# Optimization experiments

Measured on AMD Instinct MI355X. Metric: run time of the kernel, lower is better.

## Reference

```python
import jax, jax.numpy as jnp
import numpy as np
import math

B_, V_, D_, N_, H_, W_ = 4, 8, 64, 16, 32, 32
V_LIST = [0.0, 45.0, 90.0, 135.0, 180.0, 225.0, 270.0, 315.0]
GROUPS = 4
EPS = 1e-5


def _make_sample_coords():
    # Replicates F.affine_grid(align_corners=False) for fixed rotation matrices,
    # then maps normalized grid coords to input pixel coords as grid_sample does.
    xs = (np.arange(W_) + 0.5) * 2.0 / W_ - 1.0
    ys = (np.arange(H_) + 0.5) * 2.0 / H_ - 1.0
    X, Y = np.meshgrid(xs, ys)  # (H, W)
    ix_list, iy_list = [], []
    for w in V_LIST:
        a = math.radians(-w)
        c, s = math.cos(a), math.sin(a)
        gx = c * X - s * Y  # theta = [[c,-s,0],[s,c,0]]
        gy = s * X + c * Y
        ix_list.append((gx + 1.0) * W_ / 2.0 - 0.5)
        iy_list.append((gy + 1.0) * H_ / 2.0 - 0.5)
    return (jnp.asarray(np.stack(ix_list), jnp.float32),
            jnp.asarray(np.stack(iy_list), jnp.float32))

IX, IY = _make_sample_coords()  # each (V, H, W)


def _bilinear(sv, iy, ix):
    # sv: (B, D, N, H, W); iy, ix: (H, W) float sampling coords (pixel space)
    x0 = jnp.floor(ix)
    y0 = jnp.floor(iy)
    wx1 = ix - x0
    wy1 = iy - y0

    def corner(yc, xc, wgt):
        m = (yc >= 0) & (yc < H_) & (xc >= 0) & (xc < W_)  # zeros padding
        yi = jnp.clip(yc, 0, H_ - 1).astype(jnp.int32)
        xi = jnp.clip(xc, 0, W_ - 1).astype(jnp.int32)
        return sv[..., yi, xi] * jnp.where(m, wgt, 0.0)

    return (corner(y0, x0, (1.0 - wy1) * (1.0 - wx1))
            + corner(y0, x0 + 1.0, (1.0 - wy1) * wx1)
            + corner(y0 + 1.0, x0, wy1 * (1.0 - wx1))
            + corner(y0 + 1.0, x0 + 1.0, wy1 * wx1))

# vmap over the velocity axis V of s_prev and the per-velocity grids
_transport = jax.vmap(_bilinear, in_axes=(1, 0, 0), out_axes=1)


def _conv(x, w, b=None):
    y = jax.lax.conv_general_dilated(x, w, (1, 1), 'SAME',
                                     dimension_numbers=('NCHW', 'OIHW', 'NCHW'))
    if b is not None:
        y = y + b[None, :, None, None]
    return y


def _group_norm(x, w, b):
    Bn, D, H, W = x.shape
    xg = x.reshape(Bn, GROUPS, D // GROUPS, H, W)
    mu = xg.mean(axis=(2, 3, 4), keepdims=True)
    var = xg.var(axis=(2, 3, 4), keepdims=True)
    xn = ((xg - mu) * jax.lax.rsqrt(var + EPS)).reshape(Bn, D, H, W)
    return xn * w[None, :, None, None] + b[None, :, None, None]


def setup_inputs() -> dict:
    key = jax.random.key(0)
    ks = jax.random.split(key, 5)
    return {
        "u_t": jax.random.normal(ks[0], (B_, D_, H_, W_), jnp.float32),
        "s_prev": jax.random.normal(ks[1], (B_, V_, D_, N_, H_, W_), jnp.float32) * 0.1,
        "gn_w": jnp.ones((D_,), jnp.float32),
        "gn_b": jnp.zeros((D_,), jnp.float32),
        "conv_delta_w": jax.random.normal(ks[2], (D_, D_, 3, 3), jnp.float32) * 0.02,
        "conv_delta_b": jnp.zeros((D_,), jnp.float32),
        "conv_B_w": jax.random.normal(ks[3], (N_, D_, 3, 3), jnp.float32) * 0.02,
        "conv_C_w": jax.random.normal(ks[4], (N_, D_, 3, 3), jnp.float32) * 0.02,
        "log_A_real": jnp.full((D_, N_), math.log(0.5), jnp.float32),
        "D_param": jnp.ones((D_,), jnp.float32),
        "dt_bias": jnp.float32(math.log(math.e - 1.0)),
    }


def reference(u_t, s_prev, gn_w, gn_b, conv_delta_w, conv_delta_b,
              conv_B_w, conv_C_w, log_A_real, D_param, dt_bias):
    u_norm = _group_norm(u_t, gn_w, gn_b)
    delta = jax.nn.softplus(_conv(u_norm, conv_delta_w, conv_delta_b) + dt_bias)
    delta = jnp.clip(delta, 1e-4, 5.0)                               # (B,D,H,W)
    B_val = _conv(u_norm, conv_B_w)                                  # (B,N,H,W)
    C_val = _conv(u_norm, conv_C_w)                                  # (B,N,H,W)
    A = -jnp.exp(log_A_real)                                         # (D,N)
    A_bar = jnp.exp(delta[:, :, None] * A[None, :, :, None, None])   # (B,D,N,H,W)
    B_bar = delta[:, :, None] * B_val[:, None]                       # (B,D,N,H,W)
    s_trans = _transport(s_prev, IY, IX)                             # (B,V,D,N,H,W)
    s_new = A_bar[:, None] * s_trans + B_bar[:, None] * u_t[:, None, :, None]
    y_state = jnp.einsum('bvdnhw,bnhw->bvdhw', s_new, C_val)
    y_new = y_state + u_t[:, None] * D_param[None, None, :, None, None]
    return (y_new, s_new)
```

## Files before the change

kernel.cpp:

```cpp
#include <hip/hip_runtime.h>
#include <cmath>

#define FSQ 0.70710678118654752440f
__constant__ float CTAB[8] = {1.f,  FSQ, 0.f, -FSQ, -1.f, -FSQ, 0.f, FSQ};
__constant__ float STAB[8] = {0.f, -FSQ, -1.f, -FSQ,  0.f,  FSQ, 1.f, FSQ};

typedef float f4 __attribute__((ext_vector_type(4)));

__global__ __launch_bounds__(1024) void gn_kernel(const float* __restrict__ u,
                                                  const float* __restrict__ gw,
                                                  const float* __restrict__ gb,
                                                  float* __restrict__ up)
{
    int blk = blockIdx.x;
    int b = blk >> 2, g = blk & 3;
    int t = threadIdx.x;
    const float* src = u + ((size_t)(b * 64 + g * 16) << 10);
    float sum = 0.f, sq = 0.f;
    #pragma unroll
    for (int r = 0; r < 16; ++r) {
        float v = src[t + (r << 10)];
        sum += v; sq += v * v;
    }
    #pragma unroll
    for (int ofs = 32; ofs > 0; ofs >>= 1) {
        sum += __shfl_down(sum, ofs);
        sq  += __shfl_down(sq, ofs);
    }
    __shared__ float red[16], red2[16];
    int wv = t >> 6;
    if ((t & 63) == 0) { red[wv] = sum; red2[wv] = sq; }
    __syncthreads();
    float s_tot = 0.f, q_tot = 0.f;
    #pragma unroll
    for (int k = 0; k < 16; ++k) { s_tot += red[k]; q_tot += red2[k]; }
    float mu  = s_tot * (1.f / 16384.f);
    float var = q_tot * (1.f / 16384.f) - mu * mu;
    float rs  = rsqrtf(var + 1e-5f);

    float* pb = up + (size_t)(b * 64 + g * 16) * 1156;
    for (int k = t; k < 16 * 132; k += 1024) {
        int pl = k / 132, c = k - pl * 132;
        int idx;
        if (c < 34)       idx = c;
        else if (c < 68)  idx = 33 * 34 + (c - 34);
        else if (c < 100) idx = (c - 68 + 1) * 34;
        else              idx = (c - 100 + 1) * 34 + 33;
        pb[pl * 1156 + idx] = 0.f;
    }
    int y = t >> 5, x = t & 31;
    #pragma unroll
    for (int r = 0; r < 16; ++r) {
        float val = (src[t + (r << 10)] - mu) * rs * gw[g * 16 + r] + gb[g * 16 + r];
        pb[r * 1156 + (y + 1) * 34 + (x + 1)] = val;
    }
}

__global__ __launch_bounds__(256) void conv_kernel(const float* __restrict__ up,
                                                   const float* __restrict__ wd,
                                                   const float* __restrict__ bd,
                                                   const float* __restrict__ wB,
                                                   const float* __restrict__ wC,
                                                   const float* __restrict__ dtb,
                                                   float* __restrict__ delta,
                                                   float* __restrict__ Bv,
                                                   float* __restrict__ Cv)
{
    __shared__ float sin_[64 * 204];
    int blk = blockIdx.x;
    int strip = blk & 7;
    int og = (blk >> 3) % 24;
    int b = blk / 192;
    int h0 = strip * 4;
    int t = threadIdx.x;

    const float* plane = up + (size_t)b * 73984;
    for (int idx = t; idx < 13056; idx += 256) {
        int ci = idx / 204;
        int rem = idx - ci * 204;
        sin_[idx] = plane[ci * 1156 + h0 * 34 + rem];
    }
    __syncthreads();

    int o0 = og * 4;
    const float* wsel;
    if (o0 < 64)      wsel = wd + (size_t)o0 * 576;
    else if (o0 < 80) wsel = wB + (size_t)(o0 - 64) * 576;
    else              wsel = wC + (size_t)(o0 - 80) * 576;

    int half = t >> 7;
    int px = t & 127;
    int r = px >> 5, c = px & 31;
    const float* base = sin_ + r * 34 + c;

    float acc0 = 0.f, acc1 = 0.f, acc2 = 0.f, acc3 = 0.f;
    int ci0 = half * 32;
    for (int ci = ci0; ci < ci0 + 32; ++ci) {
        const float* pp = base + ci * 204;
        const float* wp = wsel + ci * 9;
        #pragma unroll
        for (int dy = 0; dy < 3; ++dy)
            #pragma unroll
            for (int dx = 0; dx < 3; ++dx) {
                float v = pp[dy * 34 + dx];
                int wi = dy * 3 + dx;
                acc0 += v * wp[wi];
                acc1 += v * wp[576 + wi];
                acc2 += v * wp[1152 + wi];
                acc3 += v * wp[1728 + wi];
            }
    }
    __syncthreads();
    float4* red4 = (float4*)sin_;
    red4[t] = make_float4(acc0, acc1, acc2, acc3);
    __syncthreads();
    if (t < 128) {
        float4 a = red4[t], bq = red4[t + 128];
        float s0 = a.x + bq.x, s1 = a.y + bq.y, s2 = a.z + bq.z, s3 = a.w + bq.w;
        float s[4] = {s0, s1, s2, s3};
        int pidx = (h0 + r) * 32 + c;
        if (o0 < 64) {
            #pragma unroll
            for (int k = 0; k < 4; ++k) {
                float x = s[k] + bd[o0 + k] + dtb[0];
                float sp = (x > 20.f) ? x : log1pf(expf(x));
                sp = fminf(fmaxf(sp, 1e-4f), 5.f);
                delta[((size_t)(b * 64 + o0 + k) << 10) + pidx] = sp;
            }
        } else if (o0 < 80) {
            #pragma unroll
            for (int k = 0; k < 4; ++k)
                Bv[((size_t)(b * 16 + o0 - 64 + k) << 10) + pidx] = s[k];
        } else {
            #pragma unroll
            for (int k = 0; k < 4; ++k)
                Cv[((size_t)(b * 16 + o0 - 80 + k) << 10) + pidx] = s[k];
        }
    }
}

__global__ __launch_bounds__(256) void fused_state_kernel(
    const float* __restrict__ s_prev, const float* __restrict__ u_t,
    const float* __restrict__ delta, const float* __restrict__ Bv,
    const float* __restrict__ Cv, const float* __restrict__ logA,
    const float* __restrict__ Dp, float* __restrict__ y_out,
    float* __restrict__ s_out)
{
    __shared__ float lds[4 * 1190];
    __shared__ float Ash[4];
    int blk = blockIdx.x;
    int cchunk = blk >> 11;
    int rest = blk & 2047;
    int d = rest & 63, v = (rest >> 6) & 7, b = rest >> 9;
    int t = threadIdx.x;

    if (t < 4) Ash[t] = -__expf(logA[d * 16 + cchunk * 4 + t]);
    for (int k = t; k < 528; k += 256) {
        int pl = k / 132, g = k - pl * 132;
        int idx;
        if (g < 34)       idx = g;
        else if (g < 68)  idx = 33 * 35 + (g - 34);
        else if (g < 100) idx = (g - 67) * 35;
        else              idx = (g - 99) * 35 + 33;
        lds[pl * 1190 + idx] = 0.f;
    }

    size_t so = (((size_t)((b * 8 + v) * 64 + d)) << 14) + ((size_t)cchunk << 12);
    const float4* src = (const float4*)(s_prev + so);
    #pragma unroll
    for (int k = 0; k < 4; ++k) {
        int q = t + (k << 8);
        float4 val = src[q];
        int lin = q << 2;
        int nn = lin >> 10, rem = lin & 1023;
        int di = nn * 1190 + ((rem >> 5) + 1) * 35 + (rem & 31) + 1;
        lds[di] = val.x; lds[di + 1] = val.y; lds[di + 2] = val.z; lds[di + 3] = val.w;
    }
    __syncthreads();

    const float cc = CTAB[v], ss = STAB[v];
    const f4* dpl4 = (const f4*)(delta + ((size_t)(b * 64 + d) << 10));
    const f4* upl4 = (const f4*)(u_t   + ((size_t)(b * 64 + d) << 10));
    const f4* bvc4 = (const f4*)(Bv + ((size_t)b << 14) + (cchunk << 12));
    const f4* cvc4 = (const f4*)(Cv + ((size_t)b << 14) + (cchunk << 12));
    f4* soc4   = (f4*)(s_out + so);
    float* yo  = y_out + (((size_t)((b * 8 + v) * 64 + d)) << 10);
    float Dd = Dp[d];

    f4 dd4 = dpl4[t], uv4 = upl4[t];

    int h = t >> 3;
    float Yc = (h + 0.5f) * 0.0625f - 1.f;
    float w00[4], w01[4], w10[4], w11[4], duv[4], yacc[4];
    int tb[4];
    #pragma unroll
    for (int j = 0; j < 4; ++j) {
        int wpx = ((t & 7) << 2) | j;
        float X = (wpx + 0.5f) * 0.0625f - 1.f;
        float gx = cc * X - ss * Yc;
        float gy = ss * X + cc * Yc;
        float ix = (gx + 1.f) * 16.f - 0.5f;
        float iy = (gy + 1.f) * 16.f - 0.5f;
        float fx0 = floorf(ix), fy0 = floorf(iy);
        float wx = ix - fx0, wy = iy - fy0;
        int x0 = (int)fx0, y0 = (int)fy0;
        float mx0 = (x0 >= 0 && x0 < 32) ? (1.f - wx) : 0.f;
        float mx1 = (x0 >= -1 && x0 < 31) ? wx : 0.f;
        float my0 = (y0 >= 0 && y0 < 32) ? (1.f - wy) : 0.f;
        float my1 = (y0 >= -1 && y0 < 31) ? wy : 0.f;
        w00[j] = my0 * mx0; w01[j] = my0 * mx1;
        w10[j] = my1 * mx0; w11[j] = my1 * mx1;
        int bx = min(max(x0, -1), 31), by = min(max(y0, -1), 31);
        tb[j] = (by + 1) * 35 + (bx + 1);
        duv[j] = dd4[j] * uv4[j];
        yacc[j] = 0.f;
    }

    #pragma unroll
    for (int nn = 0; nn < 4; ++nn) {
        f4 B4 = bvc4[(nn << 8) + t];
        f4 C4 = cvc4[(nn << 8) + t];
        f4 sn4;
        #pragma unroll
        for (int j = 0; j < 4; ++j) {
            int si = tb[j] + nn * 1190;
            float bil = lds[si] * w00[j] + lds[si + 1] * w01[j]
                      + lds[si + 35] * w10[j] + lds[si + 36] * w11[j];
            float abar = __expf(dd4[j] * Ash[nn]);
            float sn = abar * bil + duv[j] * B4[j];
            sn4[j] = sn;
            yacc[j] += sn * C4[j];
        }
        __builtin_nontemporal_store(sn4, soc4 + (nn << 8) + t);
    }

    #pragma unroll
    for (int j = 0; j < 4; ++j) {
        float val = yacc[j] + (cchunk == 0 ? uv4[j] * Dd : 0.f);
        atomicAdd(yo + (t << 2) + j, val);
    }
}

extern "C" void kernel_launch(void* const* d_in, const int* in_sizes, int n_in,
                              void* d_out, int out_size, void* d_ws, size_t ws_size,
                              hipStream_t stream)
{
    const float* u_t    = (const float*)d_in[0];
    const float* s_prev = (const float*)d_in[1];
    const float* gn_w   = (const float*)d_in[2];
    const float* gn_b   = (const float*)d_in[3];
    const float* wd     = (const float*)d_in[4];
    const float* bd     = (const float*)d_in[5];
    const float* wB     = (const float*)d_in[6];
    const float* wC     = (const float*)d_in[7];
    const float* logA   = (const float*)d_in[8];
    const float* Dp     = (const float*)d_in[9];
    const float* dtb    = (const float*)d_in[10];

    float* y_out = (float*)d_out;
    float* s_out = y_out + 2097152;

    float* up    = (float*)d_ws;
    float* delta = up + 295936;
    float* Bv    = delta + 262144;
    float* Cv    = Bv + 65536;

    hipMemsetAsync(y_out, 0, (size_t)2097152 * sizeof(float), stream);

    hipLaunchKernelGGL(gn_kernel, dim3(16), dim3(1024), 0, stream, u_t, gn_w, gn_b, up);
    hipLaunchKernelGGL(conv_kernel, dim3(768), dim3(256), 0, stream,
                       up, wd, bd, wB, wC, dtb, delta, Bv, Cv);
    hipLaunchKernelGGL(fused_state_kernel, dim3(8192), dim3(256), 0, stream,
                       s_prev, u_t, delta, Bv, Cv, logA, Dp, y_out, s_out);
}
```

Measured before the change: 355.4 us.

## Loop over N chunks per block to drop atomics and y memset

Each block now handles all 16 state channels for one (b,v,d) by looping over four chunks serially, and reuses the per-pixel bilinear weights across them. The y output is accumulated in registers and written with a single vector store, which removes the atomicAdd reduction and the separate memset of y. The price is 4x fewer blocks with serialized load/sync phases, so less latency hiding. The s_out stores also change from nontemporal to regular stores.

```diff
diff --git a/kernel.cpp b/kernel.cpp
--- a/kernel.cpp
+++ b/kernel.cpp
@@ -147,14 +147,12 @@
     float* __restrict__ s_out)
 {
     __shared__ float lds[4 * 1190];
-    __shared__ float Ash[4];
+    __shared__ float Ash[16];
     int blk = blockIdx.x;
-    int cchunk = blk >> 11;
-    int rest = blk & 2047;
-    int d = rest & 63, v = (rest >> 6) & 7, b = rest >> 9;
+    int d = blk & 63, v = (blk >> 6) & 7, b = blk >> 9;
     int t = threadIdx.x;
 
-    if (t < 4) Ash[t] = -__expf(logA[d * 16 + cchunk * 4 + t]);
+    if (t < 16) Ash[t] = -__expf(logA[d * 16 + t]);
     for (int k = t; k < 528; k += 256) {
         int pl = k / 132, g = k - pl * 132;
         int idx;
@@ -165,26 +163,10 @@
         lds[pl * 1190 + idx] = 0.f;
     }
 
-    size_t so = (((size_t)((b * 8 + v) * 64 + d)) << 14) + ((size_t)cchunk << 12);
-    const float4* src = (const float4*)(s_prev + so);
-    #pragma unroll
-    for (int k = 0; k < 4; ++k) {
-        int q = t + (k << 8);
-        float4 val = src[q];
-        int lin = q << 2;
-        int nn = lin >> 10, rem = lin & 1023;
-        int di = nn * 1190 + ((rem >> 5) + 1) * 35 + (rem & 31) + 1;
-        lds[di] = val.x; lds[di + 1] = val.y; lds[di + 2] = val.z; lds[di + 3] = val.w;
-    }
-    __syncthreads();
-
+    size_t so_base = ((size_t)((b * 8 + v) * 64 + d)) << 14;
     const float cc = CTAB[v], ss = STAB[v];
     const f4* dpl4 = (const f4*)(delta + ((size_t)(b * 64 + d) << 10));
     const f4* upl4 = (const f4*)(u_t   + ((size_t)(b * 64 + d) << 10));
-    const f4* bvc4 = (const f4*)(Bv + ((size_t)b << 14) + (cchunk << 12));
-    const f4* cvc4 = (const f4*)(Cv + ((size_t)b << 14) + (cchunk << 12));
-    f4* soc4   = (f4*)(s_out + so);
-    float* yo  = y_out + (((size_t)((b * 8 + v) * 64 + d)) << 10);
     float Dd = Dp[d];
 
     f4 dd4 = dpl4[t], uv4 = upl4[t];
@@ -216,29 +198,49 @@
         yacc[j] = 0.f;
     }
 
-    #pragma unroll
-    for (int nn = 0; nn < 4; ++nn) {
-        f4 B4 = bvc4[(nn << 8) + t];
-        f4 C4 = cvc4[(nn << 8) + t];
-        f4 sn4;
+    #pragma unroll 1
+    for (int c = 0; c < 4; ++c) {
+        if (c) __syncthreads();
+        const float4* src = (const float4*)(s_prev + so_base + ((size_t)c << 12));
         #pragma unroll
-        for (int j = 0; j < 4; ++j) {
-            int si = tb[j] + nn * 1190;
-            float bil = lds[si] * w00[j] + lds[si + 1] * w01[j]
-                      + lds[si + 35] * w10[j] + lds[si + 36] * w11[j];
-            float abar = __expf(dd4[j] * Ash[nn]);
-            float sn = abar * bil + duv[j] * B4[j];
-            sn4[j] = sn;
-            yacc[j] += sn * C4[j];
+        for (int k = 0; k < 4; ++k) {
+            int q = t + (k << 8);
+            float4 val = src[q];
+            int lin = q << 2;
+            int nn = lin >> 10, rem = lin & 1023;
+            int di = nn * 1190 + ((rem >> 5) + 1) * 35 + (rem & 31) + 1;
+            lds[di] = val.x; lds[di + 1] = val.y; lds[di + 2] = val.z; lds[di + 3] = val.w;
         }
-        __builtin_nontemporal_store(sn4, soc4 + (nn << 8) + t);
-    }
-
-    #pragma unroll
-    for (int j = 0; j < 4; ++j) {
-        float val = yacc[j] + (cchunk == 0 ? uv4[j] * Dd : 0.f);
-        atomicAdd(yo + (t << 2) + j, val);
-    }
+        __syncthreads();
+
+        const f4* bvc4 = (const f4*)(Bv + ((size_t)b << 14) + (c << 12));
+        const f4* cvc4 = (const f4*)(Cv + ((size_t)b << 14) + (c << 12));
+        f4* soc4 = (f4*)(s_out + so_base + ((size_t)c << 12));
+        #pragma unroll
+        for (int nn = 0; nn < 4; ++nn) {
+            f4 B4 = bvc4[(nn << 8) + t];
+            f4 C4 = cvc4[(nn << 8) + t];
+            float An = Ash[(c << 2) + nn];
+            f4 sn4;
+            #pragma unroll
+            for (int j = 0; j < 4; ++j) {
+                int si = tb[j] + nn * 1190;
+                float bil = lds[si] * w00[j] + lds[si + 1] * w01[j]
+                          + lds[si + 35] * w10[j] + lds[si + 36] * w11[j];
+                float abar = __expf(dd4[j] * An);
+                float sn = abar * bil + duv[j] * B4[j];
+                sn4[j] = sn;
+                yacc[j] += sn * C4[j];
+            }
+            soc4[(nn << 8) + t] = sn4;
+        }
+    }
+
+    f4 y4;
+    #pragma unroll
+    for (int j = 0; j < 4; ++j) y4[j] = yacc[j] + uv4[j] * Dd;
+    f4* yo4 = (f4*)(y_out + (((size_t)((b * 8 + v) * 64 + d)) << 10));
+    yo4[t] = y4;
 }
 
 extern "C" void kernel_launch(void* const* d_in, const int* in_sizes, int n_in,
@@ -265,11 +267,9 @@
     float* Bv    = delta + 262144;
     float* Cv    = Bv + 65536;
 
-    hipMemsetAsync(y_out, 0, (size_t)2097152 * sizeof(float), stream);
-
     hipLaunchKernelGGL(gn_kernel, dim3(16), dim3(1024), 0, stream, u_t, gn_w, gn_b, up);
     hipLaunchKernelGGL(conv_kernel, dim3(768), dim3(256), 0, stream,
                        up, wd, bd, wB, wC, dtb, delta, Bv, Cv);
-    hipLaunchKernelGGL(fused_state_kernel, dim3(8192), dim3(256), 0, stream,
+    hipLaunchKernelGGL(fused_state_kernel, dim3(2048), dim3(256), 0, stream,
                        s_prev, u_t, delta, Bv, Cv, logA, Dp, y_out, s_out);
 }
```

Result: faster. 306.1 us (-13.9%).
